# Performance work log

Measured on AMD Instinct MI355X. Metric: run time of the kernel, lower is better.

## Reference

```python
import jax, jax.numpy as jnp
import numpy as np

NPOINT, RADIUS, NSAMPLE = 1024, 0.2, 32
EPS = 1e-5


def _fps(xyz, npoint):
    # Iterative farthest point sampling (deterministic start at index 0).
    B, N, _ = xyz.shape
    def step(carry, _):
        distance, farthest = carry
        centroid = jnp.take_along_axis(xyz, farthest[:, None, None], axis=1)  # (B,1,3)
        d = jnp.sum((xyz - centroid) ** 2, -1)                                # (B,N)
        distance = jnp.minimum(distance, d)
        return (distance, jnp.argmax(distance, -1)), farthest
    init = (jnp.full((B, N), 1e10, xyz.dtype), jnp.zeros((B,), jnp.int32))
    _, idx = jax.lax.scan(step, init, None, length=npoint)
    return idx.T  # (B, npoint)


def _gather(points, idx):
    # points (B,N,C), idx (B,S,K) -> (B,S,K,C)
    B, S, K = idx.shape
    flat = jnp.take_along_axis(points, idx.reshape(B, S * K)[:, :, None], axis=1)
    return flat.reshape(B, S, K, points.shape[-1])


def _query_ball(xyz, new_xyz):
    # For each centroid, first NSAMPLE point indices within RADIUS (pad with first hit).
    B, N, _ = xyz.shape
    sqr = jnp.sum((new_xyz[:, :, None, :] - xyz[:, None, :, :]) ** 2, -1)  # (B,S,N)
    gi = jnp.where(sqr > RADIUS ** 2, N, jnp.arange(N, dtype=jnp.int32)[None, None, :])
    gi = jnp.sort(gi, axis=-1)[:, :, :NSAMPLE]
    return jnp.where(gi == N, gi[:, :, :1], gi)  # (B,S,K)


def _cond_layer(x, t_embed, wt, bt, wc, bc, g, b):
    # ConditionalConv1d: x += time_mlp(gelu(t)); 1x1 conv; BatchNorm (batch stats); GELU.
    tp = jax.nn.gelu(t_embed, approximate=False) @ wt.T + bt      # (B,Cin)
    x = x + tp[:, None, None, :]
    y = jnp.einsum('bskc,oc->bsko', x, wc) + bc                   # (B,S,K,Cout)
    mu = jnp.mean(y, axis=(0, 1, 2))
    var = jnp.var(y, axis=(0, 1, 2))
    y = (y - mu) * jax.lax.rsqrt(var + EPS) * g + b
    return jax.nn.gelu(y, approximate=False)


def _forward(xyz, points, t_embed, params):
    fps_idx = _fps(xyz, NPOINT)                                        # (B,S)
    new_xyz = jnp.take_along_axis(xyz, fps_idx[:, :, None], axis=1)    # (B,S,3)
    idx = _query_ball(xyz, new_xyz)                                    # (B,S,K)
    grouped_xyz = _gather(xyz, idx) - new_xyz[:, :, None, :]           # (B,S,K,3)
    grouped_pts = _gather(jnp.swapaxes(points, 1, 2), idx)             # (B,S,K,C)
    x = jnp.concatenate([grouped_xyz, grouped_pts], -1)                # (B,S,K,C+3)
    for p in params:
        x = _cond_layer(x, t_embed, *p)
    new_points = jnp.swapaxes(jnp.max(x, axis=2), 1, 2)                # (B,Cout,S)
    return new_xyz, new_points


def setup_inputs() -> dict:
    key = jax.random.key(0)
    ks = iter(jax.random.split(key, 32))
    B, N, CIN, T = 8, 4096, 64, 128
    chans = [(CIN + 3, 64), (64, 64), (64, 128)]
    inp = {
        "xyz": jax.random.normal(next(ks), (B, N, 3), jnp.float32),
        "points": jax.random.normal(next(ks), (B, CIN, N), jnp.float32),
        "t_embed": jax.random.normal(next(ks), (B, T), jnp.float32),
    }
    for i, (ci, co) in enumerate(chans):
        inp[f"wt{i}"] = jax.random.normal(next(ks), (ci, T), jnp.float32) * 0.05
        inp[f"bt{i}"] = jnp.zeros((ci,), jnp.float32)
        inp[f"wc{i}"] = jax.random.normal(next(ks), (co, ci), jnp.float32) * 0.1
        inp[f"bc{i}"] = jnp.zeros((co,), jnp.float32)
        inp[f"g{i}"] = jnp.ones((co,), jnp.float32)
        inp[f"be{i}"] = jnp.zeros((co,), jnp.float32)
    return inp


def reference(xyz, points, t_embed,
              wt0, bt0, wc0, bc0, g0, be0,
              wt1, bt1, wc1, bc1, g1, be1,
              wt2, bt2, wc2, bc2, g2, be2):
    params = [(wt0, bt0, wc0, bc0, g0, be0),
              (wt1, bt1, wc1, bc1, g1, be1),
              (wt2, bt2, wc2, bc2, g2, be2)]
    return _forward(xyz, points, t_embed, params)
```

## Files before the change

### kernel.cpp

```cpp
#include <hip/hip_runtime.h>
#include <cmath>

#define Bc 8
#define Nc 4096
#define Sc 1024
#define Kc 32
#define Mc (Bc*Sc*Kc)

__device__ __forceinline__ float gelu_f(float x){
  return 0.5f*x*(1.0f + erff(x*0.70710678f));
}

__global__ __launch_bounds__(256) void tp_kernel(const float* __restrict__ t_embed,
    const float* __restrict__ wt0, const float* __restrict__ bt0,
    const float* __restrict__ wt1, const float* __restrict__ bt1,
    const float* __restrict__ wt2, const float* __restrict__ bt2,
    float* __restrict__ tp){
  __shared__ float ge[Bc*128];
  const int tid = threadIdx.x;
  for (int i = tid; i < Bc*128; i += 256){
    ge[i] = gelu_f(t_embed[i]);
  }
  __syncthreads();
  for (int i = tid; i < 3*Bc*68; i += 256){
    int l = i / (Bc*68);
    int r = i - l*(Bc*68);
    int b = r / 68;
    int c = r - b*68;
    int ci = (l==0) ? 67 : 64;
    float v = 0.0f;
    if (c < ci){
      const float* wt = (l==0)?wt0:((l==1)?wt1:wt2);
      const float* bt = (l==0)?bt0:((l==1)?bt1:bt2);
      const float* w = wt + c*128;
      const float* g = ge + b*128;
      float acc = 0.0f;
      for (int t=0;t<128;++t) acc = fmaf(g[t], w[t], acc);
      v = acc + bt[c];
    }
    tp[i] = v;
  }
}

__global__ __launch_bounds__(256) void fps_kernel(const float* __restrict__ xyz,
                                                  float* __restrict__ new_xyz){
  const int b = blockIdx.x;
  const int tid = threadIdx.x;
  const int lane = tid & 63;
  const int wv = tid >> 6;
  const float* xb = xyz + b*Nc*3;
  __shared__ float sx[Nc], sy[Nc], sz[Nc];
  __shared__ unsigned long long skey[2][4];
  float px[16], py[16], pz[16], dist[16];
#pragma unroll
  for (int j=0;j<16;++j){
    const int i = tid + (j<<8);
    const float x = xb[i*3+0], y = xb[i*3+1], z = xb[i*3+2];
    px[j]=x; py[j]=y; pz[j]=z;
    sx[i]=x; sy[i]=y; sz[i]=z;
    dist[j]=1e10f;
  }
  __syncthreads();
  int widx = 0;
  for (int it=0; it<Sc; ++it){
    const float cx = sx[widx], cy = sy[widx], cz = sz[widx];
    if (tid==0){
      float* o = new_xyz + ((size_t)b*Sc + it)*3;
      o[0]=cx; o[1]=cy; o[2]=cz;
    }
    float bv = -1.0f; int bj = 0;
#pragma unroll
    for (int j=0;j<16;++j){
      const float dx=__fsub_rn(px[j],cx);
      const float dy=__fsub_rn(py[j],cy);
      const float dz=__fsub_rn(pz[j],cz);
      const float dd=__fadd_rn(__fadd_rn(__fmul_rn(dx,dx),__fmul_rn(dy,dy)),__fmul_rn(dz,dz));
      const float dn=fminf(dist[j],dd);
      dist[j]=dn;
      if (dn > bv){ bv=dn; bj=j; }
    }
    const int bidx = tid + (bj<<8);
    unsigned long long key = ((unsigned long long)__float_as_uint(bv) << 32)
                           | (unsigned long long)(unsigned int)(4095 - bidx);
#pragma unroll
    for (int off=1; off<64; off<<=1){
      const unsigned long long ok = __shfl_xor(key, off);
      key = (ok > key) ? ok : key;
    }
    const int p = it & 1;
    if (lane==0) skey[p][wv] = key;
    __syncthreads();
    const unsigned long long k0 = skey[p][0];
    const unsigned long long k1 = skey[p][1];
    const unsigned long long k2 = skey[p][2];
    const unsigned long long k3 = skey[p][3];
    unsigned long long ka = (k0>k1)?k0:k1;
    unsigned long long kb = (k2>k3)?k2:k3;
    ka = (ka>kb)?ka:kb;
    widx = 4095 - (int)(unsigned int)(ka & 0xFFFFFFFFull);
  }
}

__global__ __launch_bounds__(256) void transpose_kernel(const float* __restrict__ points,
                                                        float* __restrict__ pointsT){
  const int b = blockIdx.y;
  const int n0 = blockIdx.x << 6;
  __shared__ float tile[64][65];
  const int tid = threadIdx.x;
  const int sub = tid >> 6;
  const int ln  = tid & 63;
#pragma unroll 4
  for (int cp=0; cp<16; ++cp){
    int c = (cp<<2) + sub;
    tile[c][ln] = points[((size_t)(b*64+c))*Nc + n0 + ln];
  }
  __syncthreads();
#pragma unroll 4
  for (int np=0; np<16; ++np){
    int nl = (np<<2) + sub;
    pointsT[((size_t)(b*Nc + n0 + nl))*64 + ln] = tile[ln][nl];
  }
}

__global__ __launch_bounds__(256) void ball_kernel(const float* __restrict__ xyz,
    const float* __restrict__ new_xyz, int* __restrict__ ballidx){
  const int g = (blockIdx.x<<2) + (threadIdx.x>>6);
  const int lane = threadIdx.x & 63;
  const int w = threadIdx.x >> 6;
  const int b = g >> 10;
  const float* xb = xyz + b*Nc*3;
  const float cx = new_xyz[g*3+0];
  const float cy = new_xyz[g*3+1];
  const float cz = new_xyz[g*3+2];
  __shared__ int sidx[4][32];
  int total = 0;
  for (int base=0; base<Nc; base+=64){
    const int i = base + lane;
    float dx=__fsub_rn(cx, xb[i*3+0]);
    float dy=__fsub_rn(cy, xb[i*3+1]);
    float dz=__fsub_rn(cz, xb[i*3+2]);
    float sq=__fadd_rn(__fadd_rn(__fmul_rn(dx,dx),__fmul_rn(dy,dy)),__fmul_rn(dz,dz));
    bool hit = !(sq > 0.04f);
    unsigned long long m = __ballot(hit);
    if (hit){
      int pos = total + (int)__popcll(m & ((1ull<<lane)-1ull));
      if (pos < 32) sidx[w][pos] = i;
    }
    total += (int)__popcll(m);
    if (total >= 32) break;
  }
  __syncthreads();
  const int fill = (total < 32) ? total : 32;
  const int first = sidx[w][0];
  if (lane >= fill && lane < 32) sidx[w][lane] = first;
  if (lane < 32) ballidx[(g<<5)+lane] = sidx[w][lane];
}

__global__ __launch_bounds__(256) void gather_kernel(const float* __restrict__ xyz,
    const float* __restrict__ new_xyz, const float* __restrict__ pointsT,
    const int* __restrict__ ballidx, float* __restrict__ X){
  const int bs = blockIdx.x;
  const int b = bs >> 10;
  const int w = threadIdx.x >> 6;
  const int lane = threadIdx.x & 63;
  const float cx=new_xyz[bs*3+0], cy=new_xyz[bs*3+1], cz=new_xyz[bs*3+2];
  for (int k=w; k<32; k+=4){
    const int pidx = ballidx[(bs<<5)+k];
    const float* pt = pointsT + ((size_t)((b<<12)+pidx))*64;
    const float* xp = xyz + ((size_t)((b<<12)+pidx))*3;
    float* xr = X + (size_t)((bs<<5)+k)*68;
    float v;
    if      (lane==0) v = __fsub_rn(xp[0], cx);
    else if (lane==1) v = __fsub_rn(xp[1], cy);
    else if (lane==2) v = __fsub_rn(xp[2], cz);
    else              v = pt[lane-3];
    xr[lane] = v;
    if (lane < 4){
      int c = 64 + lane;
      xr[c] = (c<67) ? pt[c-3] : 0.0f;
    }
  }
}

template<int CI_REAL, int CI_PAD, int LDX>
__global__ __launch_bounds__(256) void mm_kernel(const float* __restrict__ X,
    const float* __restrict__ wc, const float* __restrict__ tp,
    float* __restrict__ Y, float* __restrict__ pS, float* __restrict__ pQ, int o_base)
{
  __shared__ __align__(16) float wT[CI_PAD][64];
  __shared__ __align__(16) float tpr[CI_PAD];
  __shared__ float redS[4][64];
  __shared__ float redQ[4][64];
  const int tid = threadIdx.x;
  const int m0 = blockIdx.x << 8;
  const int b  = blockIdx.x >> 7;
  for (int idx = tid; idx < CI_PAD*64; idx += 256){
    int c = idx >> 6, o = idx & 63;
    wT[c][o] = (c < CI_REAL) ? wc[(o_base + o)*CI_REAL + c] : 0.0f;
  }
  if (tid < CI_PAD) tpr[tid] = tp[b*68 + tid];
  __syncthreads();
  const int rg = tid >> 2, cg = tid & 3;
  const float* x0 = X + (size_t)(m0 + (rg<<2)) * LDX;
  float4 acc[4][4];
#pragma unroll
  for (int r=0;r<4;++r)
#pragma unroll
    for (int q=0;q<4;++q) acc[r][q] = make_float4(0.f,0.f,0.f,0.f);

  for (int c = 0; c < CI_PAD; c += 4){
    const float4 tpv = *reinterpret_cast<const float4*>(&tpr[c]);
    float4 xr[4];
#pragma unroll
    for (int r=0;r<4;++r){
      float4 xv = *reinterpret_cast<const float4*>(x0 + r*LDX + c);
      xr[r] = make_float4(xv.x+tpv.x, xv.y+tpv.y, xv.z+tpv.z, xv.w+tpv.w);
    }
#pragma unroll
    for (int cc=0; cc<4; ++cc){
      const float* wrow = &wT[c+cc][cg<<4];
      const float4 w0 = *reinterpret_cast<const float4*>(wrow);
      const float4 w1 = *reinterpret_cast<const float4*>(wrow+4);
      const float4 w2 = *reinterpret_cast<const float4*>(wrow+8);
      const float4 w3 = *reinterpret_cast<const float4*>(wrow+12);
#pragma unroll
      for (int r=0;r<4;++r){
        const float xs = (cc==0)?xr[r].x:((cc==1)?xr[r].y:((cc==2)?xr[r].z:xr[r].w));
        acc[r][0].x = fmaf(xs, w0.x, acc[r][0].x);
        acc[r][0].y = fmaf(xs, w0.y, acc[r][0].y);
        acc[r][0].z = fmaf(xs, w0.z, acc[r][0].z);
        acc[r][0].w = fmaf(xs, w0.w, acc[r][0].w);
        acc[r][1].x = fmaf(xs, w1.x, acc[r][1].x);
        acc[r][1].y = fmaf(xs, w1.y, acc[r][1].y);
        acc[r][1].z = fmaf(xs, w1.z, acc[r][1].z);
        acc[r][1].w = fmaf(xs, w1.w, acc[r][1].w);
        acc[r][2].x = fmaf(xs, w2.x, acc[r][2].x);
        acc[r][2].y = fmaf(xs, w2.y, acc[r][2].y);
        acc[r][2].z = fmaf(xs, w2.z, acc[r][2].z);
        acc[r][2].w = fmaf(xs, w2.w, acc[r][2].w);
        acc[r][3].x = fmaf(xs, w3.x, acc[r][3].x);
        acc[r][3].y = fmaf(xs, w3.y, acc[r][3].y);
        acc[r][3].z = fmaf(xs, w3.z, acc[r][3].z);
        acc[r][3].w = fmaf(xs, w3.w, acc[r][3].w);
      }
    }
  }
#pragma unroll
  for (int r=0;r<4;++r){
    float4* yp = reinterpret_cast<float4*>(Y + (size_t)(m0 + (rg<<2) + r)*64 + (cg<<4));
#pragma unroll
    for (int q=0;q<4;++q) yp[q] = acc[r][q];
  }
  float4 s[4], q2[4];
#pragma unroll
  for (int q=0;q<4;++q){
    float sx=0,sy=0,sz=0,sw=0, qx=0,qy=0,qz=0,qw=0;
#pragma unroll
    for (int r=0;r<4;++r){
      sx+=acc[r][q].x; qx+=acc[r][q].x*acc[r][q].x;
      sy+=acc[r][q].y; qy+=acc[r][q].y*acc[r][q].y;
      sz+=acc[r][q].z; qz+=acc[r][q].z*acc[r][q].z;
      sw+=acc[r][q].w; qw+=acc[r][q].w*acc[r][q].w;
    }
    s[q]=make_float4(sx,sy,sz,sw); q2[q]=make_float4(qx,qy,qz,qw);
  }
  const int lane = tid & 63, wvv = tid >> 6;
#pragma unroll
  for (int off=32; off>=4; off>>=1){
#pragma unroll
    for (int q=0;q<4;++q){
      s[q].x  += __shfl_down(s[q].x,  off);
      s[q].y  += __shfl_down(s[q].y,  off);
      s[q].z  += __shfl_down(s[q].z,  off);
      s[q].w  += __shfl_down(s[q].w,  off);
      q2[q].x += __shfl_down(q2[q].x, off);
      q2[q].y += __shfl_down(q2[q].y, off);
      q2[q].z += __shfl_down(q2[q].z, off);
      q2[q].w += __shfl_down(q2[q].w, off);
    }
  }
  if (lane < 4){
#pragma unroll
    for (int q=0;q<4;++q){
      redS[wvv][lane*16 + q*4 + 0] = s[q].x;
      redS[wvv][lane*16 + q*4 + 1] = s[q].y;
      redS[wvv][lane*16 + q*4 + 2] = s[q].z;
      redS[wvv][lane*16 + q*4 + 3] = s[q].w;
      redQ[wvv][lane*16 + q*4 + 0] = q2[q].x;
      redQ[wvv][lane*16 + q*4 + 1] = q2[q].y;
      redQ[wvv][lane*16 + q*4 + 2] = q2[q].z;
      redQ[wvv][lane*16 + q*4 + 3] = q2[q].w;
    }
  }
  __syncthreads();
  if (tid < 64){
    float a=0.f, bb=0.f;
#pragma unroll
    for (int w2=0; w2<4; ++w2){ a += redS[w2][tid]; bb += redQ[w2][tid]; }
    pS[(blockIdx.x<<6) + tid] = a;
    pQ[(blockIdx.x<<6) + tid] = bb;
  }
}

__global__ __launch_bounds__(256) void finalize_kernel(const float* __restrict__ pS,
    const float* __restrict__ pQ, const float* __restrict__ g, const float* __restrict__ be,
    float* __restrict__ scale, float* __restrict__ shift, int nblk){
  __shared__ float rS[4][64], rQ[4][64];
  const int o = threadIdx.x & 63;
  const int ch = threadIdx.x >> 6;
  const int per = nblk >> 2;
  float s=0.f, q=0.f;
  const int i0 = ch*per;
#pragma unroll 4
  for (int i=0;i<per;++i){
    s += pS[((i0+i)<<6)+o];
    q += pQ[((i0+i)<<6)+o];
  }
  rS[ch][o]=s; rQ[ch][o]=q;
  __syncthreads();
  if (threadIdx.x < 64){
    float ss = rS[0][o]+rS[1][o]+rS[2][o]+rS[3][o];
    float qq = rQ[0][o]+rQ[1][o]+rQ[2][o]+rQ[3][o];
    const float inv_n = 1.0f/(float)Mc;
    const float mu = ss*inv_n;
    const float var = qq*inv_n - mu*mu;
    const float rs = 1.0f/sqrtf(var + 1e-5f);
    const float sc = rs*g[o];
    scale[o] = sc;
    shift[o] = fmaf(-mu, sc, be[o]);
  }
}

__global__ __launch_bounds__(256) void norm_kernel(const float4* __restrict__ Y,
    const float* __restrict__ scale, const float* __restrict__ shift,
    float4* __restrict__ Xo, int n4){
  int i = blockIdx.x*blockDim.x + threadIdx.x;
  const int stride = gridDim.x*blockDim.x;
  for (; i<n4; i+=stride){
    const int c = (i & 15) << 2;
    const float4 sc = *reinterpret_cast<const float4*>(scale + c);
    const float4 sh = *reinterpret_cast<const float4*>(shift + c);
    float4 y = Y[i];
    float4 o;
    o.x = gelu_f(fmaf(y.x, sc.x, sh.x));
    o.y = gelu_f(fmaf(y.y, sc.y, sh.y));
    o.z = gelu_f(fmaf(y.z, sc.z, sh.z));
    o.w = gelu_f(fmaf(y.w, sc.w, sh.w));
    Xo[i] = o;
  }
}

__global__ __launch_bounds__(256) void pool_kernel(const float* __restrict__ Y,
    const float* __restrict__ scale, const float* __restrict__ shift,
    float* __restrict__ out, int o_base){
  __shared__ float pool[32][65];
  const int tid = threadIdx.x;
  const int b  = blockIdx.x >> 5;
  const int s0 = (blockIdx.x & 31) << 5;
  const int c  = tid & 63;
  const int sl0 = tid >> 6;
  const float sc = scale[c], sh = shift[c];
  for (int sp=0; sp<8; ++sp){
    const int sl = (sp<<2) + sl0;
    const int s = s0 + sl;
    const float* yp = Y + ((size_t)((b<<10)+s)<<5)*64 + c;
    float mx = -1e30f;
#pragma unroll 4
    for (int k=0;k<32;++k){
      float v = yp[(size_t)(k<<6)];
      v = gelu_f(fmaf(v, sc, sh));
      mx = fmaxf(mx, v);
    }
    pool[sl][c] = mx;
  }
  __syncthreads();
  for (int p=0;p<8;++p){
    const int c2 = (p<<3) + (tid>>5);
    const int sl = tid & 31;
    out[((size_t)((b<<7) + o_base + c2)<<10) + s0 + sl] = pool[sl][c2];
  }
}

extern "C" void kernel_launch(void* const* d_in, const int* in_sizes, int n_in,
                              void* d_out, int out_size, void* d_ws, size_t ws_size,
                              hipStream_t stream){
  const float* xyz     = (const float*)d_in[0];
  const float* points  = (const float*)d_in[1];
  const float* t_embed = (const float*)d_in[2];
  const float* wt0=(const float*)d_in[3],  *bt0=(const float*)d_in[4],  *wc0=(const float*)d_in[5];
  const float* g0 =(const float*)d_in[7],  *be0=(const float*)d_in[8];
  const float* wt1=(const float*)d_in[9],  *bt1=(const float*)d_in[10], *wc1=(const float*)d_in[11];
  const float* g1 =(const float*)d_in[13], *be1=(const float*)d_in[14];
  const float* wt2=(const float*)d_in[15], *bt2=(const float*)d_in[16], *wc2=(const float*)d_in[17];
  const float* g2 =(const float*)d_in[19], *be2=(const float*)d_in[20];

  float* out_xyz = (float*)d_out;
  float* out_pts = (float*)d_out + Bc*Sc*3;

  float* ws       = (float*)d_ws;
  float* tp       = ws + 0;
  float* pointsT  = ws + 2048;
  int*   ballidx  = (int*)(ws + 2099200);
  float* X        = ws + 2361344;
  float* Y        = ws + 20187136;
  float* pS       = ws + 36964352;
  float* pQ       = ws + 37029888;
  float* scale    = ws + 37095424;
  float* shift    = ws + 37095488;

  tp_kernel<<<1, 256, 0, stream>>>(t_embed, wt0,bt0, wt1,bt1, wt2,bt2, tp);
  fps_kernel<<<Bc, 256, 0, stream>>>(xyz, out_xyz);
  transpose_kernel<<<dim3(64, Bc), 256, 0, stream>>>(points, pointsT);
  ball_kernel<<<(Bc*Sc)/4, 256, 0, stream>>>(xyz, out_xyz, ballidx);
  gather_kernel<<<Bc*Sc, 256, 0, stream>>>(xyz, out_xyz, pointsT, ballidx, X);

  mm_kernel<67,68,68><<<Mc/256, 256, 0, stream>>>(X, wc0, tp, Y, pS, pQ, 0);
  finalize_kernel<<<1, 256, 0, stream>>>(pS, pQ, g0, be0, scale, shift, Mc/256);
  norm_kernel<<<4096, 256, 0, stream>>>((const float4*)Y, scale, shift, (float4*)X, Mc*64/4);

  mm_kernel<64,64,64><<<Mc/256, 256, 0, stream>>>(X, wc1, tp + 544, Y, pS, pQ, 0);
  finalize_kernel<<<1, 256, 0, stream>>>(pS, pQ, g1, be1, scale, shift, Mc/256);
  norm_kernel<<<4096, 256, 0, stream>>>((const float4*)Y, scale, shift, (float4*)X, Mc*64/4);

  mm_kernel<64,64,64><<<Mc/256, 256, 0, stream>>>(X, wc2, tp + 1088, Y, pS, pQ, 0);
  finalize_kernel<<<1, 256, 0, stream>>>(pS, pQ, g2, be2, scale, shift, Mc/256);
  pool_kernel<<<Bc*Sc/32, 256, 0, stream>>>(Y, scale, shift, out_pts, 0);

  mm_kernel<64,64,64><<<Mc/256, 256, 0, stream>>>(X, wc2, tp + 1088, Y, pS, pQ, 64);
  finalize_kernel<<<1, 256, 0, stream>>>(pS, pQ, g2+64, be2+64, scale, shift, Mc/256);
  pool_kernel<<<Bc*Sc/32, 256, 0, stream>>>(Y, scale, shift, out_pts, 64);
}
```

Measured before the change: 1.319 ms.

## Use packed FP32 math and DPP two-pass argmax reduction in FPS kernel

The farthest point sampling loop now computes distances with packed v_pk_add/v_pk_mul on pairs of points. The 64-bit shuffle-based argmax is replaced by a 32-bit DPP max reduction followed by a DPP min-index reduction over the lanes matching the max. The cross-wave step reads both values with vectorised shared loads. This targets the serial per-iteration reduction latency of the FPS loop, which is the critical path, at the cost of an extra pass over the distances and reliance on exact float equality for tie-breaking.

After: 1.312 ms. Within noise of the previous version (-0.6%).

```diff
diff --git a/kernel.cpp b/kernel.cpp
--- a/kernel.cpp
+++ b/kernel.cpp
@@ -7,9 +7,31 @@
 #define Kc 32
 #define Mc (Bc*Sc*Kc)
 
+typedef float v2f __attribute__((ext_vector_type(2)));
+
 __device__ __forceinline__ float gelu_f(float x){
   return 0.5f*x*(1.0f + erff(x*0.70710678f));
 }
+
+__device__ __forceinline__ v2f pk_add(v2f a, v2f b){
+  v2f d; asm("v_pk_add_f32 %0, %1, %2" : "=v"(d) : "v"(a), "v"(b)); return d;
+}
+__device__ __forceinline__ v2f pk_mul(v2f a, v2f b){
+  v2f d; asm("v_pk_mul_f32 %0, %1, %2" : "=v"(d) : "v"(a), "v"(b)); return d;
+}
+
+#define ROR_MAXF(v, n) { int _t = __builtin_amdgcn_update_dpp(__float_as_int(v), __float_as_int(v), 0x120|(n), 0xF, 0xF, false); \
+                         v = fmaxf(v, __int_as_float(_t)); }
+#define BC15_MAXF(v)   { int _t = __builtin_amdgcn_update_dpp(__float_as_int(v), __float_as_int(v), 0x142, 0xA, 0xF, false); \
+                         v = fmaxf(v, __int_as_float(_t)); }
+#define BC31_MAXF(v)   { int _t = __builtin_amdgcn_update_dpp(__float_as_int(v), __float_as_int(v), 0x143, 0xC, 0xF, false); \
+                         v = fmaxf(v, __int_as_float(_t)); }
+#define ROR_MINU(v, n) { unsigned _t = (unsigned)__builtin_amdgcn_update_dpp((int)(v), (int)(v), 0x120|(n), 0xF, 0xF, false); \
+                         v = (v < _t) ? v : _t; }
+#define BC15_MINU(v)   { unsigned _t = (unsigned)__builtin_amdgcn_update_dpp((int)(v), (int)(v), 0x142, 0xA, 0xF, false); \
+                         v = (v < _t) ? v : _t; }
+#define BC31_MINU(v)   { unsigned _t = (unsigned)__builtin_amdgcn_update_dpp((int)(v), (int)(v), 0x143, 0xC, 0xF, false); \
+                         v = (v < _t) ? v : _t; }
 
 __global__ __launch_bounds__(256) void tp_kernel(const float* __restrict__ t_embed,
     const float* __restrict__ wt0, const float* __restrict__ bt0,
@@ -50,54 +72,73 @@
   const int wv = tid >> 6;
   const float* xb = xyz + b*Nc*3;
   __shared__ float sx[Nc], sy[Nc], sz[Nc];
-  __shared__ unsigned long long skey[2][4];
-  float px[16], py[16], pz[16], dist[16];
-#pragma unroll
-  for (int j=0;j<16;++j){
-    const int i = tid + (j<<8);
-    const float x = xb[i*3+0], y = xb[i*3+1], z = xb[i*3+2];
-    px[j]=x; py[j]=y; pz[j]=z;
-    sx[i]=x; sy[i]=y; sz[i]=z;
-    dist[j]=1e10f;
+  __shared__ __align__(16) float    sMV[2][4];
+  __shared__ __align__(16) unsigned sIV[2][4];
+  v2f px2[8], py2[8], pz2[8], dist2[8];
+#pragma unroll
+  for (int k=0;k<8;++k){
+    const int i0 = tid + (2*k)*256;
+    const int i1 = tid + (2*k+1)*256;
+    const float x0=xb[i0*3+0], y0=xb[i0*3+1], z0=xb[i0*3+2];
+    const float x1=xb[i1*3+0], y1=xb[i1*3+1], z1=xb[i1*3+2];
+    px2[k].x=x0; px2[k].y=x1; py2[k].x=y0; py2[k].y=y1; pz2[k].x=z0; pz2[k].y=z1;
+    sx[i0]=x0; sy[i0]=y0; sz[i0]=z0;
+    sx[i1]=x1; sy[i1]=y1; sz[i1]=z1;
+    dist2[k].x=1e10f; dist2[k].y=1e10f;
   }
   __syncthreads();
   int widx = 0;
   for (int it=0; it<Sc; ++it){
-    const float cx = sx[widx], cy = sy[widx], cz = sz[widx];
+    const float cx=sx[widx], cy=sy[widx], cz=sz[widx];
     if (tid==0){
       float* o = new_xyz + ((size_t)b*Sc + it)*3;
       o[0]=cx; o[1]=cy; o[2]=cz;
     }
-    float bv = -1.0f; int bj = 0;
-#pragma unroll
-    for (int j=0;j<16;++j){
-      const float dx=__fsub_rn(px[j],cx);
-      const float dy=__fsub_rn(py[j],cy);
-      const float dz=__fsub_rn(pz[j],cz);
-      const float dd=__fadd_rn(__fadd_rn(__fmul_rn(dx,dx),__fmul_rn(dy,dy)),__fmul_rn(dz,dz));
-      const float dn=fminf(dist[j],dd);
-      dist[j]=dn;
-      if (dn > bv){ bv=dn; bj=j; }
-    }
-    const int bidx = tid + (bj<<8);
-    unsigned long long key = ((unsigned long long)__float_as_uint(bv) << 32)
-                           | (unsigned long long)(unsigned int)(4095 - bidx);
-#pragma unroll
-    for (int off=1; off<64; off<<=1){
-      const unsigned long long ok = __shfl_xor(key, off);
-      key = (ok > key) ? ok : key;
-    }
+    v2f ncx, ncy, ncz;
+    ncx.x=-cx; ncx.y=-cx; ncy.x=-cy; ncy.y=-cy; ncz.x=-cz; ncz.y=-cz;
+    float bvx=-1.0f, bvy=-1.0f;
+#pragma unroll
+    for (int k=0;k<8;++k){
+      const v2f dx = pk_add(px2[k], ncx);
+      const v2f dy = pk_add(py2[k], ncy);
+      const v2f dz = pk_add(pz2[k], ncz);
+      const v2f dd = pk_add(pk_add(pk_mul(dx,dx), pk_mul(dy,dy)), pk_mul(dz,dz));
+      v2f dn;
+      dn.x = fminf(dist2[k].x, dd.x);
+      dn.y = fminf(dist2[k].y, dd.y);
+      dist2[k] = dn;
+      bvx = fmaxf(bvx, dn.x);
+      bvy = fmaxf(bvy, dn.y);
+    }
+    float mv = fmaxf(bvx, bvy);
+    ROR_MAXF(mv,1); ROR_MAXF(mv,2); ROR_MAXF(mv,4); ROR_MAXF(mv,8);
+    BC15_MAXF(mv); BC31_MAXF(mv);
+    mv = __int_as_float(__builtin_amdgcn_readlane(__float_as_int(mv), 63));
+    unsigned iv = 0xFFFFFFFFu;
+#pragma unroll
+    for (int k=0;k<8;++k){
+      const unsigned c0 = (dist2[k].x == mv) ? (unsigned)(tid + (2*k  )*256) : 0xFFFFFFFFu;
+      const unsigned c1 = (dist2[k].y == mv) ? (unsigned)(tid + (2*k+1)*256) : 0xFFFFFFFFu;
+      iv = (iv < c0) ? iv : c0;
+      iv = (iv < c1) ? iv : c1;
+    }
+    ROR_MINU(iv,1); ROR_MINU(iv,2); ROR_MINU(iv,4); ROR_MINU(iv,8);
+    BC15_MINU(iv); BC31_MINU(iv);
+    iv = (unsigned)__builtin_amdgcn_readlane((int)iv, 63);
     const int p = it & 1;
-    if (lane==0) skey[p][wv] = key;
+    if (lane==0){ sMV[p][wv] = mv; sIV[p][wv] = iv; }
     __syncthreads();
-    const unsigned long long k0 = skey[p][0];
-    const unsigned long long k1 = skey[p][1];
-    const unsigned long long k2 = skey[p][2];
-    const unsigned long long k3 = skey[p][3];
-    unsigned long long ka = (k0>k1)?k0:k1;
-    unsigned long long kb = (k2>k3)?k2:k3;
-    ka = (ka>kb)?ka:kb;
-    widx = 4095 - (int)(unsigned int)(ka & 0xFFFFFFFFull);
+    const float4 m4 = *reinterpret_cast<const float4*>(&sMV[p][0]);
+    const uint4  i4 = *reinterpret_cast<const uint4*>(&sIV[p][0]);
+    const float bm = fmaxf(fmaxf(m4.x,m4.y), fmaxf(m4.z,m4.w));
+    const unsigned v0 = (m4.x==bm)? i4.x : 0xFFFFFFFFu;
+    const unsigned v1 = (m4.y==bm)? i4.y : 0xFFFFFFFFu;
+    const unsigned v2 = (m4.z==bm)? i4.z : 0xFFFFFFFFu;
+    const unsigned v3 = (m4.w==bm)? i4.w : 0xFFFFFFFFu;
+    unsigned wmin = (v0<v1)?v0:v1;
+    const unsigned wmin2 = (v2<v3)?v2:v3;
+    wmin = (wmin<wmin2)?wmin:wmin2;
+    widx = (int)wmin;
   }
 }
 
```

## Fuse FPS/transpose/time-MLP into one launch and fold BN+GELU into matmul input

Applied to the files above, without the earlier changes.

FPS, the points transpose and the time-MLP projection are merged into one kernel launch, with each role picked by block index. FPS now runs 512 threads per batch and uses packed f32 math plus a DPP-based argmax reduction, and it writes the sampled coordinates once at the end from an index history. The standalone norm_kernel passes are removed: BatchNorm scale/shift and GELU are applied while the next mm_kernel loads its input. The two halves of layer 2 go to separate buffers so that both pool kernels can run after both finalizes. This cuts full-tensor memory passes and launch count, at the cost of recomputing GELU inside the matmul (for the final layer, twice) and an in-place Y read/write that depends on each block touching only its own rows.

Result: slower. 1.685 ms (+27.7%).

```diff
diff --git a/kernel.cpp b/kernel.cpp
--- a/kernel.cpp
+++ b/kernel.cpp
@@ -7,118 +7,157 @@
 #define Kc 32
 #define Mc (Bc*Sc*Kc)
 
+typedef float v2f __attribute__((ext_vector_type(2)));
+
 __device__ __forceinline__ float gelu_f(float x){
   return 0.5f*x*(1.0f + erff(x*0.70710678f));
 }
 
-__global__ __launch_bounds__(256) void tp_kernel(const float* __restrict__ t_embed,
+__device__ __forceinline__ v2f pk_add(v2f a, v2f b){
+  v2f d; asm("v_pk_add_f32 %0, %1, %2" : "=v"(d) : "v"(a), "v"(b)); return d;
+}
+__device__ __forceinline__ v2f pk_mul(v2f a, v2f b){
+  v2f d; asm("v_pk_mul_f32 %0, %1, %2" : "=v"(d) : "v"(a), "v"(b)); return d;
+}
+
+#define DPP_ARG_STEP(ctrl, rmask) { \
+  const float  _tv = __int_as_float(__builtin_amdgcn_update_dpp(__float_as_int(bv), __float_as_int(bv), (ctrl), (rmask), 0xF, false)); \
+  const unsigned _ti = (unsigned)__builtin_amdgcn_update_dpp((int)bi, (int)bi, (ctrl), (rmask), 0xF, false); \
+  const bool _tk = (_tv > bv) || ((_tv == bv) && (_ti < bi)); \
+  bv = _tk ? _tv : bv; bi = _tk ? _ti : bi; }
+
+#define TK(v_, i_) { const bool _t = ((v_) > Bv) || (((v_) == Bv) && ((i_) < Bi)); \
+  Bv = _t ? (v_) : Bv; Bi = _t ? (i_) : Bi; }
+
+__global__ __launch_bounds__(512) void fused_front_kernel(
+    const float* __restrict__ xyz, float* __restrict__ new_xyz,
+    const float* __restrict__ points, float* __restrict__ pointsT,
+    const float* __restrict__ t_embed,
     const float* __restrict__ wt0, const float* __restrict__ bt0,
     const float* __restrict__ wt1, const float* __restrict__ bt1,
     const float* __restrict__ wt2, const float* __restrict__ bt2,
-    float* __restrict__ tp){
-  __shared__ float ge[Bc*128];
+    float* __restrict__ tp)
+{
+  __shared__ __align__(16) float smem[Nc*4 + 16 + 16 + 1024];
+  const int bid = blockIdx.x;
   const int tid = threadIdx.x;
-  for (int i = tid; i < Bc*128; i += 256){
-    ge[i] = gelu_f(t_embed[i]);
-  }
-  __syncthreads();
-  for (int i = tid; i < 3*Bc*68; i += 256){
-    int l = i / (Bc*68);
-    int r = i - l*(Bc*68);
-    int b = r / 68;
-    int c = r - b*68;
-    int ci = (l==0) ? 67 : 64;
-    float v = 0.0f;
-    if (c < ci){
-      const float* wt = (l==0)?wt0:((l==1)?wt1:wt2);
-      const float* bt = (l==0)?bt0:((l==1)?bt1:bt2);
-      const float* w = wt + c*128;
-      const float* g = ge + b*128;
-      float acc = 0.0f;
-      for (int t=0;t<128;++t) acc = fmaf(g[t], w[t], acc);
-      v = acc + bt[c];
-    }
-    tp[i] = v;
-  }
-}
-
-__global__ __launch_bounds__(256) void fps_kernel(const float* __restrict__ xyz,
-                                                  float* __restrict__ new_xyz){
-  const int b = blockIdx.x;
-  const int tid = threadIdx.x;
-  const int lane = tid & 63;
-  const int wv = tid >> 6;
-  const float* xb = xyz + b*Nc*3;
-  __shared__ float sx[Nc], sy[Nc], sz[Nc];
-  __shared__ unsigned long long skey[2][4];
-  float px[16], py[16], pz[16], dist[16];
-#pragma unroll
-  for (int j=0;j<16;++j){
-    const int i = tid + (j<<8);
-    const float x = xb[i*3+0], y = xb[i*3+1], z = xb[i*3+2];
-    px[j]=x; py[j]=y; pz[j]=z;
-    sx[i]=x; sy[i]=y; sz[i]=z;
-    dist[j]=1e10f;
-  }
-  __syncthreads();
-  int widx = 0;
-  for (int it=0; it<Sc; ++it){
-    const float cx = sx[widx], cy = sy[widx], cz = sz[widx];
-    if (tid==0){
-      float* o = new_xyz + ((size_t)b*Sc + it)*3;
-      o[0]=cx; o[1]=cy; o[2]=cz;
-    }
-    float bv = -1.0f; int bj = 0;
-#pragma unroll
-    for (int j=0;j<16;++j){
-      const float dx=__fsub_rn(px[j],cx);
-      const float dy=__fsub_rn(py[j],cy);
-      const float dz=__fsub_rn(pz[j],cz);
-      const float dd=__fadd_rn(__fadd_rn(__fmul_rn(dx,dx),__fmul_rn(dy,dy)),__fmul_rn(dz,dz));
-      const float dn=fminf(dist[j],dd);
-      dist[j]=dn;
-      if (dn > bv){ bv=dn; bj=j; }
-    }
-    const int bidx = tid + (bj<<8);
-    unsigned long long key = ((unsigned long long)__float_as_uint(bv) << 32)
-                           | (unsigned long long)(unsigned int)(4095 - bidx);
-#pragma unroll
-    for (int off=1; off<64; off<<=1){
-      const unsigned long long ok = __shfl_xor(key, off);
-      key = (ok > key) ? ok : key;
-    }
-    const int p = it & 1;
-    if (lane==0) skey[p][wv] = key;
+
+  if (bid < 8){
+    const int b = bid;
+    const int lane = tid & 63;
+    const int wv = tid >> 6;
+    const float* xb = xyz + b*Nc*3;
+    float4*   c4    = (float4*)smem;
+    float*    skv   = smem + Nc*4;
+    unsigned* ski   = (unsigned*)(smem + Nc*4 + 16);
+    int*      shist = (int*)(smem + Nc*4 + 32);
+
+    v2f px2[4], py2[4], pz2[4], d2[4];
+#pragma unroll
+    for (int k=0;k<4;++k){
+      const int i0 = tid + (2*k)*512;
+      const int i1 = tid + (2*k+1)*512;
+      const float x0=xb[i0*3+0], y0=xb[i0*3+1], z0=xb[i0*3+2];
+      const float x1=xb[i1*3+0], y1=xb[i1*3+1], z1=xb[i1*3+2];
+      px2[k].x=x0; px2[k].y=x1; py2[k].x=y0; py2[k].y=y1; pz2[k].x=z0; pz2[k].y=z1;
+      c4[i0] = make_float4(x0,y0,z0,0.f);
+      c4[i1] = make_float4(x1,y1,z1,0.f);
+      d2[k].x=1e10f; d2[k].y=1e10f;
+    }
     __syncthreads();
-    const unsigned long long k0 = skey[p][0];
-    const unsigned long long k1 = skey[p][1];
-    const unsigned long long k2 = skey[p][2];
-    const unsigned long long k3 = skey[p][3];
-    unsigned long long ka = (k0>k1)?k0:k1;
-    unsigned long long kb = (k2>k3)?k2:k3;
-    ka = (ka>kb)?ka:kb;
-    widx = 4095 - (int)(unsigned int)(ka & 0xFFFFFFFFull);
-  }
-}
-
-__global__ __launch_bounds__(256) void transpose_kernel(const float* __restrict__ points,
-                                                        float* __restrict__ pointsT){
-  const int b = blockIdx.y;
-  const int n0 = blockIdx.x << 6;
-  __shared__ float tile[64][65];
-  const int tid = threadIdx.x;
-  const int sub = tid >> 6;
-  const int ln  = tid & 63;
-#pragma unroll 4
-  for (int cp=0; cp<16; ++cp){
-    int c = (cp<<2) + sub;
-    tile[c][ln] = points[((size_t)(b*64+c))*Nc + n0 + ln];
-  }
-  __syncthreads();
-#pragma unroll 4
-  for (int np=0; np<16; ++np){
-    int nl = (np<<2) + sub;
-    pointsT[((size_t)(b*Nc + n0 + nl))*64 + ln] = tile[ln][nl];
+    int widx = 0;
+    for (int it=0; it<Sc; ++it){
+      const float4 cc = c4[widx];
+      if (tid==0) shist[it] = widx;
+      v2f ncx, ncy, ncz;
+      ncx.x=-cc.x; ncx.y=-cc.x; ncy.x=-cc.y; ncy.y=-cc.y; ncz.x=-cc.z; ncz.y=-cc.z;
+      float bvx=-1.0f, bvy=-1.0f;
+#pragma unroll
+      for (int k=0;k<4;++k){
+        const v2f dx = pk_add(px2[k], ncx);
+        const v2f dy = pk_add(py2[k], ncy);
+        const v2f dz = pk_add(pz2[k], ncz);
+        const v2f dd = pk_add(pk_add(pk_mul(dx,dx), pk_mul(dy,dy)), pk_mul(dz,dz));
+        v2f dn;
+        dn.x = fminf(d2[k].x, dd.x);
+        dn.y = fminf(d2[k].y, dd.y);
+        d2[k] = dn;
+        bvx = fmaxf(bvx, dn.x);
+        bvy = fmaxf(bvy, dn.y);
+      }
+      float bv = fmaxf(bvx, bvy);
+      unsigned bi = 0xFFFFFFFFu;
+#pragma unroll
+      for (int k=0;k<4;++k){
+        const unsigned c0 = (d2[k].x == bv) ? (unsigned)(tid + (2*k  )*512) : 0xFFFFFFFFu;
+        const unsigned c1 = (d2[k].y == bv) ? (unsigned)(tid + (2*k+1)*512) : 0xFFFFFFFFu;
+        const unsigned cm = (c0 < c1) ? c0 : c1;
+        bi = (cm < bi) ? cm : bi;
+      }
+      DPP_ARG_STEP(0x121, 0xF)
+      DPP_ARG_STEP(0x122, 0xF)
+      DPP_ARG_STEP(0x124, 0xF)
+      DPP_ARG_STEP(0x128, 0xF)
+      DPP_ARG_STEP(0x142, 0xA)
+      DPP_ARG_STEP(0x143, 0xC)
+      const int p8 = (it & 1) << 3;
+      if (lane==63){ skv[p8+wv] = bv; ski[p8+wv] = bi; }
+      __syncthreads();
+      const float4 va = *reinterpret_cast<const float4*>(&skv[p8]);
+      const float4 vb = *reinterpret_cast<const float4*>(&skv[p8+4]);
+      const uint4  ia = *reinterpret_cast<const uint4*>(&ski[p8]);
+      const uint4  ib = *reinterpret_cast<const uint4*>(&ski[p8+4]);
+      float Bv = va.x; unsigned Bi = ia.x;
+      TK(va.y, ia.y) TK(va.z, ia.z) TK(va.w, ia.w)
+      TK(vb.x, ib.x) TK(vb.y, ib.y) TK(vb.z, ib.z) TK(vb.w, ib.w)
+      widx = (int)Bi;
+    }
+    __syncthreads();
+    for (int i = tid; i < Sc; i += 512){
+      const float4 cc = c4[shist[i]];
+      float* o = new_xyz + ((size_t)b*Sc + i)*3;
+      o[0]=cc.x; o[1]=cc.y; o[2]=cc.z;
+    }
+  } else if (bid < 520){
+    const int t  = bid - 8;
+    const int tb = t >> 6;
+    const int n0 = (t & 63) << 6;
+    float (*tile)[65] = (float(*)[65])smem;
+    const int sub = tid >> 6;
+    const int ln  = tid & 63;
+#pragma unroll
+    for (int cp=0; cp<8; ++cp){
+      const int c = (cp<<3) + sub;
+      tile[c][ln] = points[((size_t)(tb*64+c))*Nc + n0 + ln];
+    }
+    __syncthreads();
+#pragma unroll
+    for (int np=0; np<8; ++np){
+      const int nl = (np<<3) + sub;
+      pointsT[((size_t)(tb*Nc + n0 + nl))*64 + ln] = tile[ln][nl];
+    }
+  } else {
+    float* ge = smem;
+    for (int i = tid; i < Bc*128; i += 512) ge[i] = gelu_f(t_embed[i]);
+    __syncthreads();
+    for (int i = tid; i < 3*Bc*68; i += 512){
+      const int l = i / (Bc*68);
+      const int r = i - l*(Bc*68);
+      const int b = r / 68;
+      const int c = r - b*68;
+      const int ci = (l==0) ? 67 : 64;
+      float v = 0.0f;
+      if (c < ci){
+        const float* wt = (l==0)?wt0:((l==1)?wt1:wt2);
+        const float* bt = (l==0)?bt0:((l==1)?bt1:bt2);
+        const float* w = wt + c*128;
+        const float* g = ge + b*128;
+        float acc = 0.0f;
+        for (int t2=0;t2<128;++t2) acc = fmaf(g[t2], w[t2], acc);
+        v = acc + bt[c];
+      }
+      tp[i] = v;
+    }
   }
 }
 
@@ -182,13 +221,15 @@
   }
 }
 
-template<int CI_REAL, int CI_PAD, int LDX>
-__global__ __launch_bounds__(256) void mm_kernel(const float* __restrict__ X,
+template<int NORMIN, int CI_REAL, int CI_PAD, int LDX>
+__global__ __launch_bounds__(256) void mm_kernel(const float* X,
     const float* __restrict__ wc, const float* __restrict__ tp,
-    float* __restrict__ Y, float* __restrict__ pS, float* __restrict__ pQ, int o_base)
+    const float* __restrict__ sc_in, const float* __restrict__ sh_in,
+    float* Y, float* __restrict__ pS, float* __restrict__ pQ, int o_base)
 {
   __shared__ __align__(16) float wT[CI_PAD][64];
   __shared__ __align__(16) float tpr[CI_PAD];
+  __shared__ __align__(16) float scN[64], shN[64];
   __shared__ float redS[4][64];
   __shared__ float redQ[4][64];
   const int tid = threadIdx.x;
@@ -199,6 +240,7 @@
     wT[c][o] = (c < CI_REAL) ? wc[(o_base + o)*CI_REAL + c] : 0.0f;
   }
   if (tid < CI_PAD) tpr[tid] = tp[b*68 + tid];
+  if (NORMIN && tid < 64){ scN[tid] = sc_in[tid]; shN[tid] = sh_in[tid]; }
   __syncthreads();
   const int rg = tid >> 2, cg = tid & 3;
   const float* x0 = X + (size_t)(m0 + (rg<<2)) * LDX;
@@ -210,10 +252,21 @@
 
   for (int c = 0; c < CI_PAD; c += 4){
     const float4 tpv = *reinterpret_cast<const float4*>(&tpr[c]);
+    float4 sci, shi;
+    if (NORMIN){
+      sci = *reinterpret_cast<const float4*>(&scN[c]);
+      shi = *reinterpret_cast<const float4*>(&shN[c]);
+    }
     float4 xr[4];
 #pragma unroll
     for (int r=0;r<4;++r){
       float4 xv = *reinterpret_cast<const float4*>(x0 + r*LDX + c);
+      if (NORMIN){
+        xv.x = gelu_f(fmaf(xv.x, sci.x, shi.x));
+        xv.y = gelu_f(fmaf(xv.y, sci.y, shi.y));
+        xv.z = gelu_f(fmaf(xv.z, sci.z, shi.z));
+        xv.w = gelu_f(fmaf(xv.w, sci.w, shi.w));
+      }
       xr[r] = make_float4(xv.x+tpv.x, xv.y+tpv.y, xv.z+tpv.z, xv.w+tpv.w);
     }
 #pragma unroll
@@ -328,25 +381,6 @@
     const float sc = rs*g[o];
     scale[o] = sc;
     shift[o] = fmaf(-mu, sc, be[o]);
-  }
-}
-
-__global__ __launch_bounds__(256) void norm_kernel(const float4* __restrict__ Y,
-    const float* __restrict__ scale, const float* __restrict__ shift,
-    float4* __restrict__ Xo, int n4){
-  int i = blockIdx.x*blockDim.x + threadIdx.x;
-  const int stride = gridDim.x*blockDim.x;
-  for (; i<n4; i+=stride){
-    const int c = (i & 15) << 2;
-    const float4 sc = *reinterpret_cast<const float4*>(scale + c);
-    const float4 sh = *reinterpret_cast<const float4*>(shift + c);
-    float4 y = Y[i];
-    float4 o;
-    o.x = gelu_f(fmaf(y.x, sc.x, sh.x));
-    o.y = gelu_f(fmaf(y.y, sc.y, sh.y));
-    o.z = gelu_f(fmaf(y.z, sc.z, sh.z));
-    o.w = gelu_f(fmaf(y.w, sc.w, sh.w));
-    Xo[i] = o;
   }
 }
 
@@ -402,31 +436,37 @@
   float* pointsT  = ws + 2048;
   int*   ballidx  = (int*)(ws + 2099200);
   float* X        = ws + 2361344;
-  float* Y        = ws + 20187136;
-  float* pS       = ws + 36964352;
-  float* pQ       = ws + 37029888;
-  float* scale    = ws + 37095424;
-  float* shift    = ws + 37095488;
-
-  tp_kernel<<<1, 256, 0, stream>>>(t_embed, wt0,bt0, wt1,bt1, wt2,bt2, tp);
-  fps_kernel<<<Bc, 256, 0, stream>>>(xyz, out_xyz);
-  transpose_kernel<<<dim3(64, Bc), 256, 0, stream>>>(points, pointsT);
+  float* Ya       = ws + 20187136;
+  float* pS0      = ws + 36964352;
+  float* pQ0      = ws + 37029888;
+  float* pS1      = ws + 37095424;
+  float* pQ1      = ws + 37160960;
+  float* sc0      = ws + 37226496;
+  float* sh0      = sc0 + 64;
+  float* sc1      = sc0 + 128;
+  float* sh1      = sc0 + 192;
+  float* sc2      = sc0 + 256;
+  float* sh2      = sc0 + 320;
+  float* sc3      = sc0 + 384;
+  float* sh3      = sc0 + 448;
+  float* Yx       = X;
+
+  fused_front_kernel<<<521, 512, 0, stream>>>(xyz, out_xyz, points, pointsT,
+      t_embed, wt0,bt0, wt1,bt1, wt2,bt2, tp);
   ball_kernel<<<(Bc*Sc)/4, 256, 0, stream>>>(xyz, out_xyz, ballidx);
   gather_kernel<<<Bc*Sc, 256, 0, stream>>>(xyz, out_xyz, pointsT, ballidx, X);
 
-  mm_kernel<67,68,68><<<Mc/256, 256, 0, stream>>>(X, wc0, tp, Y, pS, pQ, 0);
-  finalize_kernel<<<1, 256, 0, stream>>>(pS, pQ, g0, be0, scale, shift, Mc/256);
-  norm_kernel<<<4096, 256, 0, stream>>>((const float4*)Y, scale, shift, (float4*)X, Mc*64/4);
-
-  mm_kernel<64,64,64><<<Mc/256, 256, 0, stream>>>(X, wc1, tp + 544, Y, pS, pQ, 0);
-  finalize_kernel<<<1, 256, 0, stream>>>(pS, pQ, g1, be1, scale, shift, Mc/256);
-  norm_kernel<<<4096, 256, 0, stream>>>((const float4*)Y, scale, shift, (float4*)X, Mc*64/4);
-
-  mm_kernel<64,64,64><<<Mc/256, 256, 0, stream>>>(X, wc2, tp + 1088, Y, pS, pQ, 0);
-  finalize_kernel<<<1, 256, 0, stream>>>(pS, pQ, g2, be2, scale, shift, Mc/256);
-  pool_kernel<<<Bc*Sc/32, 256, 0, stream>>>(Y, scale, shift, out_pts, 0);
-
-  mm_kernel<64,64,64><<<Mc/256, 256, 0, stream>>>(X, wc2, tp + 1088, Y, pS, pQ, 64);
-  finalize_kernel<<<1, 256, 0, stream>>>(pS, pQ, g2+64, be2+64, scale, shift, Mc/256);
-  pool_kernel<<<Bc*Sc/32, 256, 0, stream>>>(Y, scale, shift, out_pts, 64);
-}
+  mm_kernel<0,67,68,68><<<Mc/256, 256, 0, stream>>>(X, wc0, tp, nullptr, nullptr, Ya, pS0, pQ0, 0);
+  finalize_kernel<<<1, 256, 0, stream>>>(pS0, pQ0, g0, be0, sc0, sh0, Mc/256);
+
+  mm_kernel<1,64,64,64><<<Mc/256, 256, 0, stream>>>(Ya, wc1, tp + 544, sc0, sh0, Ya, pS0, pQ0, 0);
+  finalize_kernel<<<1, 256, 0, stream>>>(pS0, pQ0, g1, be1, sc1, sh1, Mc/256);
+
+  mm_kernel<1,64,64,64><<<Mc/256, 256, 0, stream>>>(Ya, wc2, tp + 1088, sc1, sh1, Yx, pS0, pQ0, 0);
+  mm_kernel<1,64,64,64><<<Mc/256, 256, 0, stream>>>(Ya, wc2, tp + 1088, sc1, sh1, Ya, pS1, pQ1, 64);
+  finalize_kernel<<<1, 256, 0, stream>>>(pS0, pQ0, g2,    be2,    sc2, sh2, Mc/256);
+  finalize_kernel<<<1, 256, 0, stream>>>(pS1, pQ1, g2+64, be2+64, sc3, sh3, Mc/256);
+
+  pool_kernel<<<Bc*Sc/32, 256, 0, stream>>>(Yx, sc2, sh2, out_pts, 0);
+  pool_kernel<<<Bc*Sc/32, 256, 0, stream>>>(Ya, sc3, sh3, out_pts, 64);
+}
```
